# Performance work log

Hardware: AMD Instinct MI355X
Metric: run time of the kernel (lower is better)

Reference implementation:

```python
import jax, jax.numpy as jnp
import numpy as np


def setup_inputs() -> dict:
    key = jax.random.key(0)
    ks = jax.random.split(key, 6)
    B_, S, D_in, D_out, R, E = 4, 2048, 2048, 2048, 64, 16
    x = jax.random.normal(ks[0], (B_, S, D_in), dtype=jnp.float32)
    W_base = jax.random.normal(ks[1], (D_out, D_in), dtype=jnp.float32) * (D_in ** -0.5)
    b_base = jax.random.normal(ks[2], (D_out,), dtype=jnp.float32) * 0.02
    # orthogonal rows, as get_orthogonal_matrix(reservoir_size, in_features)
    G = np.asarray(jax.random.normal(ks[3], (D_in, R), dtype=jnp.float32))
    Q, _ = np.linalg.qr(G)  # [D_in, R] orthonormal columns
    A = jnp.asarray(Q.T, dtype=jnp.float32)  # [R, D_in]
    # B initialized to zeros in the module; use small random so delta is nontrivial
    Bmat = jax.random.normal(ks[4], (E, D_out, R), dtype=jnp.float32) * 0.02
    W_router = jax.random.normal(ks[5], (E, D_in), dtype=jnp.float32) * 0.02
    return {"x": x, "W_base": W_base, "b_base": b_base, "A": A, "B": Bmat,
            "W_router": W_router, "top_k": 2}


def reference(x, W_base, b_base, A, B, W_router, top_k):
    E = W_router.shape[0]
    base_output = jnp.einsum('bsi,oi->bso', x, W_base) + b_base          # [B,S,D_out]
    res_hidden = jnp.einsum('bsi,ri->bsr', x, A)                          # [B,S,R]
    router_logits = jnp.einsum('bsi,ei->bse', x, W_router)                # [B,S,E]
    routing_weights = jax.nn.softmax(router_logits, axis=-1)
    if top_k > 0 and top_k < E:
        _, top_idx = jax.lax.top_k(routing_weights, top_k)                # [B,S,k]
        mask = jax.nn.one_hot(top_idx, E, dtype=routing_weights.dtype).sum(axis=-2)
        routing_weights = routing_weights * mask
        routing_weights = routing_weights / (routing_weights.sum(axis=-1, keepdims=True) + 1e-6)
    # contract experts+rank without materializing [B,S,E,D_out]
    h = jnp.einsum('bsr,bse->bser', res_hidden, routing_weights)          # [B,S,E,R] (small)
    delta = jnp.einsum('bser,edr->bsd', h, B)                             # [B,S,D_out]
    return base_output + delta
```

## Files before the change

### kernel.cpp

```cpp
#include <hip/hip_runtime.h>
#include <hip/hip_bf16.h>

#define D_IN  2048
#define D_OUT 2048
#define RNK   64
#define NE    16
#define KTOT  3072

typedef __attribute__((ext_vector_type(8))) short bf16x8;
typedef __attribute__((ext_vector_type(4))) float f32x4;

__device__ __forceinline__ void async_ld16(const void* g, void* l) {
    __builtin_amdgcn_global_load_lds(
        (const __attribute__((address_space(1))) void*)g,
        (__attribute__((address_space(3))) void*)l,
        16, 0, 0);
}

__global__ __launch_bounds__(384) void castwa_kernel(
    const float* __restrict__ Wb, const float* __restrict__ Bm,
    const float* __restrict__ A,
    __hip_bfloat16* __restrict__ Wc, __hip_bfloat16* __restrict__ Ab)
{
    const int c = threadIdx.x * 8;
    const float* src;
    __hip_bfloat16* dst;
    if (blockIdx.x < D_OUT) {
        const int n = blockIdx.x;
        if (c < D_IN) {
            src = Wb + (size_t)n * D_IN + c;
        } else {
            const int j = c - D_IN;
            const int e = j >> 6, r = j & 63;
            src = Bm + ((size_t)e * D_OUT + n) * RNK + r;
        }
        dst = Wc + (size_t)n * KTOT + c;
    } else {
        if (c >= D_IN) return;
        const int r = blockIdx.x - D_OUT;
        src = A + (size_t)r * D_IN + c;
        dst = Ab + (size_t)r * D_IN + c;
    }
    const float4 a = *(const float4*)src;
    const float4 b = *(const float4*)(src + 4);
    const float vv[8] = {a.x, a.y, a.z, a.w, b.x, b.y, b.z, b.w};
    union { bf16x8 v; __hip_bfloat16 h[8]; } u;
#pragma unroll
    for (int q = 0; q < 8; ++q) u.h[q] = __float2bfloat16(vv[q]);
    *(bf16x8*)dst = u.v;
}

__global__ __launch_bounds__(256) void prep_kernel(
    const float* __restrict__ x, const float* __restrict__ Wr,
    const int* __restrict__ topk_p, __hip_bfloat16* __restrict__ Xc,
    float* __restrict__ wfin)
{
    __shared__ __align__(16) float wr_lds[2][NE * 256];
    const int tid = threadIdx.x;
    const int wave = tid >> 6, lane = tid & 63;
    const int t0 = blockIdx.x * 8 + wave * 2;

    float acc[NE][2];
#pragma unroll
    for (int e = 0; e < NE; ++e) { acc[e][0] = 0.f; acc[e][1] = 0.f; }

    const float4* x4 = (const float4*)x;

    auto stage = [&](int buf, int i) {
#pragma unroll
        for (int j = 0; j < 4; ++j) {
            const int r = wave * 4 + j;
            async_ld16(Wr + (size_t)r * D_IN + i * 256 + lane * 4,
                       (void*)&wr_lds[buf][r * 256]);
        }
    };

    stage(0, 0);
    __syncthreads();

#pragma unroll
    for (int i = 0; i < 8; ++i) {
        if (i < 7) stage((i + 1) & 1, i + 1);

        float4 xv[2];
#pragma unroll
        for (int t = 0; t < 2; ++t) {
            xv[t] = x4[(size_t)(t0 + t) * 512 + i * 64 + lane];
            union { short4 v; __hip_bfloat16 h[4]; } u;
            u.h[0] = __float2bfloat16(xv[t].x); u.h[1] = __float2bfloat16(xv[t].y);
            u.h[2] = __float2bfloat16(xv[t].z); u.h[3] = __float2bfloat16(xv[t].w);
            *(short4*)(Xc + (size_t)(t0 + t) * KTOT + (i * 64 + lane) * 4) = u.v;
        }

        const float4* wr4 = (const float4*)wr_lds[i & 1];
#pragma unroll
        for (int e = 0; e < NE; ++e) {
            const float4 wv = wr4[e * 64 + lane];
#pragma unroll
            for (int t = 0; t < 2; ++t)
                acc[e][t] += xv[t].x * wv.x + xv[t].y * wv.y
                           + xv[t].z * wv.z + xv[t].w * wv.w;
        }
        __syncthreads();
    }

#pragma unroll
    for (int off = 32; off; off >>= 1)
#pragma unroll
        for (int e = 0; e < NE; ++e)
#pragma unroll
            for (int t = 0; t < 2; ++t)
                acc[e][t] += __shfl_xor(acc[e][t], off, 64);

    if (lane < 2) {
        const int tt = lane;
        const int k = topk_p[0];
        float m = -1e30f;
#pragma unroll
        for (int e = 0; e < NE; ++e) m = fmaxf(m, acc[e][tt]);
        float w[NE]; float ssum = 0.f;
#pragma unroll
        for (int e = 0; e < NE; ++e) { w[e] = __expf(acc[e][tt] - m); ssum += w[e]; }
        const float inv = 1.f / ssum;
#pragma unroll
        for (int e = 0; e < NE; ++e) w[e] *= inv;
        float* wfout = wfin + (size_t)(t0 + tt) * NE;
        if (k > 0 && k < NE) {
            int chosen[NE];
#pragma unroll
            for (int e = 0; e < NE; ++e) chosen[e] = 0;
            float ksum = 0.f;
            for (int it = 0; it < k; ++it) {
                int bi = 0; float bv = -1.f;
                for (int e = 0; e < NE; ++e)
                    if (!chosen[e] && w[e] > bv) { bv = w[e]; bi = e; }
                chosen[bi] = 1; ksum += bv;
            }
            const float rinv = 1.f / (ksum + 1e-6f);
            for (int e = 0; e < NE; ++e) wfout[e] = chosen[e] ? w[e] * rinv : 0.f;
        } else {
            for (int e = 0; e < NE; ++e) wfout[e] = w[e];
        }
    }
}

__global__ __launch_bounds__(256) void rhfused_kernel(
    __hip_bfloat16* Xc, const __hip_bfloat16* __restrict__ Ab,
    const float* __restrict__ wfin)
{
    __shared__ __align__(16) char smem[10240 + 1024];
    __hip_bfloat16* lds_a = (__hip_bfloat16*)smem;
    __hip_bfloat16* lds_b = (__hip_bfloat16*)(smem + 2048);
    const int tid = threadIdx.x;
    const int wave = tid >> 6, lane = tid & 63;
    const int qm = lane & 15, quad = lane >> 4;
    const int ar = lane >> 3;
    const int ac = ((lane & 7) ^ ar) * 8;
    const int t0b = blockIdx.x * 16;

    f32x4 acc = {};

    for (int k0 = 0; k0 < D_IN; k0 += 64) {
        if (wave < 2) {
            const __hip_bfloat16* ga =
                Xc + (size_t)(t0b + wave * 8 + ar) * KTOT + k0 + ac;
            async_ld16(ga, (void*)&lds_a[wave * 512]);
        }
#pragma unroll
        for (int j = 0; j < 2; ++j) {
            const __hip_bfloat16* gb =
                Ab + (size_t)(wave * 16 + j * 8 + ar) * D_IN + k0 + ac;
            async_ld16(gb, (void*)&lds_b[(wave * 2 + j) * 512]);
        }
        __syncthreads();
#pragma unroll
        for (int kk = 0; kk < 64; kk += 32) {
            const int cg = (kk >> 3) + quad;
            const int sw = (cg ^ (qm & 7)) * 8;
            bf16x8 af = *(const bf16x8*)&lds_a[qm * 64 + sw];
            bf16x8 bfr = *(const bf16x8*)&lds_b[(wave * 16 + qm) * 64 + sw];
            acc = __builtin_amdgcn_mfma_f32_16x16x32_bf16(af, bfr, acc, 0, 0, 0);
        }
        __syncthreads();
    }

    float* rh = (float*)smem;
    float* wf = (float*)(smem + 4096);
#pragma unroll
    for (int r = 0; r < 4; ++r)
        rh[(quad * 4 + r) * 64 + wave * 16 + qm] = acc[r];
    if (tid < 64) {
        const int t = tid >> 2, part = tid & 3;
        ((float4*)wf)[t * 4 + part] =
            ((const float4*)(wfin + (size_t)(t0b + t) * NE))[part];
    }
    __syncthreads();

#pragma unroll
    for (int it = 0; it < 8; ++it) {
        const int s = it * 256 + tid;
        const int t = s >> 7;
        const int chunk = s & 127;
        const int e = chunk >> 3, r0 = (chunk & 7) * 8;
        const float w = wf[t * 16 + e];
        union { bf16x8 v; __hip_bfloat16 h[8]; } u;
#pragma unroll
        for (int q = 0; q < 8; ++q)
            u.h[q] = __float2bfloat16(w * rh[t * 64 + r0 + q]);
        *(bf16x8*)(Xc + (size_t)(t0b + t) * KTOT + D_IN + chunk * 8) = u.v;
    }
}

__global__ __launch_bounds__(256) void gemm_kernel(
    const __hip_bfloat16* __restrict__ Am,
    const __hip_bfloat16* __restrict__ Bm,
    const float* __restrict__ bias,
    float* __restrict__ C, int M, int N)
{
    __shared__ __hip_bfloat16 lds_a[128 * 64];
    __shared__ __hip_bfloat16 lds_b[128 * 64];
    const int tid = threadIdx.x;
    const int wave = tid >> 6, lane = tid & 63;
    const int bm = blockIdx.x, bn = blockIdx.y;
    const int qm = lane & 15, quad = lane >> 4;
    const int ar = lane >> 3;
    const int ac = ((lane & 7) ^ ar) * 8;

    f32x4 acc[4][4] = {};
    const int wm = (wave >> 1) * 64, wn = (wave & 1) * 64;

    const __hip_bfloat16* ga[4];
    const __hip_bfloat16* gb[4];
#pragma unroll
    for (int j = 0; j < 4; ++j) {
        ga[j] = Am + (size_t)(bm * 128 + wave * 32 + j * 8 + ar) * KTOT + ac;
        gb[j] = Bm + (size_t)(bn * 128 + wave * 32 + j * 8 + ar) * KTOT + ac;
    }

    for (int k0 = 0; k0 < KTOT; k0 += 64) {
#pragma unroll
        for (int j = 0; j < 4; ++j) {
            async_ld16(ga[j], (void*)&lds_a[(wave * 4 + j) * 512]);
            async_ld16(gb[j], (void*)&lds_b[(wave * 4 + j) * 512]);
            ga[j] += 64; gb[j] += 64;
        }
        __syncthreads();

#pragma unroll
        for (int kk = 0; kk < 64; kk += 32) {
            const int cg = (kk >> 3) + quad;
            const int sw = (cg ^ (qm & 7)) * 8;
            bf16x8 af[4], bfr[4];
#pragma unroll
            for (int i = 0; i < 4; ++i)
                af[i] = *(const bf16x8*)&lds_a[(wm + i * 16 + qm) * 64 + sw];
#pragma unroll
            for (int j = 0; j < 4; ++j)
                bfr[j] = *(const bf16x8*)&lds_b[(wn + j * 16 + qm) * 64 + sw];
#pragma unroll
            for (int i = 0; i < 4; ++i)
#pragma unroll
                for (int j = 0; j < 4; ++j)
                    acc[i][j] = __builtin_amdgcn_mfma_f32_16x16x32_bf16(
                        af[i], bfr[j], acc[i][j], 0, 0, 0);
        }
        __syncthreads();
    }

    const size_t row0 = (size_t)bm * 128 + wm;
    const int col0 = bn * 128 + wn;
#pragma unroll
    for (int j = 0; j < 4; ++j) {
        const int col = col0 + j * 16 + qm;
        const float bb = bias[col];
#pragma unroll
        for (int i = 0; i < 4; ++i) {
#pragma unroll
            for (int r = 0; r < 4; ++r) {
                const size_t row = row0 + i * 16 + quad * 4 + r;
                C[row * (size_t)N + col] = acc[i][j][r] + bb;
            }
        }
    }
}

extern "C" void kernel_launch(void* const* d_in, const int* in_sizes, int n_in,
                              void* d_out, int out_size, void* d_ws, size_t ws_size,
                              hipStream_t stream) {
    const float* x    = (const float*)d_in[0];
    const float* Wb   = (const float*)d_in[1];
    const float* bb   = (const float*)d_in[2];
    const float* A    = (const float*)d_in[3];
    const float* Bm   = (const float*)d_in[4];
    const float* Wr   = (const float*)d_in[5];
    const int*   topk = (const int*)d_in[6];
    float* out = (float*)d_out;
    const int T = in_sizes[0] / D_IN;

    __hip_bfloat16* Xc = (__hip_bfloat16*)d_ws;
    __hip_bfloat16* Wc = (__hip_bfloat16*)((char*)d_ws + (size_t)T * KTOT * 2);
    __hip_bfloat16* Ab = (__hip_bfloat16*)d_out;
    float* wfin = (float*)d_out + 8 * 1024 * 1024;

    castwa_kernel<<<D_OUT + RNK, 384, 0, stream>>>(Wb, Bm, A, Wc, Ab);
    prep_kernel<<<T / 8, 256, 0, stream>>>(x, Wr, topk, Xc, wfin);
    rhfused_kernel<<<T / 16, 256, 0, stream>>>(Xc, Ab, wfin);
    gemm_kernel<<<dim3(T / 128, D_OUT / 128), 256, 0, stream>>>(Xc, Wc, bb, out, T, D_OUT);
}
```

Before: 302.4 us.

## Split-K rh kernel across waves with direct global loads and LDS reduction

The res_hidden kernel now gives each wave a quarter of the K dimension and has it compute all 64 rank columns. Operands are loaded straight from global memory into registers, replacing the async LDS staging and the two barriers per K step. The four partial results are then summed through LDS before the routing weights are applied. This removes most synchronisation and gives more MFMA work per load, at the cost of more register pressure and uncoalesced 16-byte global reads of the A matrix by every block.

```diff
diff --git a/kernel.cpp b/kernel.cpp
--- a/kernel.cpp
+++ b/kernel.cpp
@@ -148,52 +148,45 @@
     __hip_bfloat16* Xc, const __hip_bfloat16* __restrict__ Ab,
     const float* __restrict__ wfin)
 {
-    __shared__ __align__(16) char smem[10240 + 1024];
-    __hip_bfloat16* lds_a = (__hip_bfloat16*)smem;
-    __hip_bfloat16* lds_b = (__hip_bfloat16*)(smem + 2048);
+    __shared__ __align__(16) float red[4][16][64];
+    __shared__ __align__(16) float wf[16 * 16];
     const int tid = threadIdx.x;
     const int wave = tid >> 6, lane = tid & 63;
     const int qm = lane & 15, quad = lane >> 4;
-    const int ar = lane >> 3;
-    const int ac = ((lane & 7) ^ ar) * 8;
-    const int t0b = blockIdx.x * 16;
-
-    f32x4 acc = {};
-
-    for (int k0 = 0; k0 < D_IN; k0 += 64) {
-        if (wave < 2) {
-            const __hip_bfloat16* ga =
-                Xc + (size_t)(t0b + wave * 8 + ar) * KTOT + k0 + ac;
-            async_ld16(ga, (void*)&lds_a[wave * 512]);
-        }
-#pragma unroll
-        for (int j = 0; j < 2; ++j) {
-            const __hip_bfloat16* gb =
-                Ab + (size_t)(wave * 16 + j * 8 + ar) * D_IN + k0 + ac;
-            async_ld16(gb, (void*)&lds_b[(wave * 2 + j) * 512]);
-        }
-        __syncthreads();
-#pragma unroll
-        for (int kk = 0; kk < 64; kk += 32) {
-            const int cg = (kk >> 3) + quad;
-            const int sw = (cg ^ (qm & 7)) * 8;
-            bf16x8 af = *(const bf16x8*)&lds_a[qm * 64 + sw];
-            bf16x8 bfr = *(const bf16x8*)&lds_b[(wave * 16 + qm) * 64 + sw];
-            acc = __builtin_amdgcn_mfma_f32_16x16x32_bf16(af, bfr, acc, 0, 0, 0);
-        }
-        __syncthreads();
-    }
-
-    float* rh = (float*)smem;
-    float* wf = (float*)(smem + 4096);
-#pragma unroll
-    for (int r = 0; r < 4; ++r)
-        rh[(quad * 4 + r) * 64 + wave * 16 + qm] = acc[r];
-    if (tid < 64) {
-        const int t = tid >> 2, part = tid & 3;
-        ((float4*)wf)[t * 4 + part] =
-            ((const float4*)(wfin + (size_t)(t0b + t) * NE))[part];
-    }
+    const int t0 = blockIdx.x * 16;
+
+    const __hip_bfloat16* xrow =
+        Xc + (size_t)(t0 + qm) * KTOT + wave * 512 + quad * 8;
+    const __hip_bfloat16* brow =
+        Ab + (size_t)qm * D_IN + wave * 512 + quad * 8;
+
+    f32x4 acc[4] = {};
+#pragma unroll
+    for (int s = 0; s < 8; ++s) {
+        const bf16x8 a0 = *(const bf16x8*)(xrow);
+        const bf16x8 a1 = *(const bf16x8*)(xrow + 32);
+        bf16x8 b0[4], b1[4];
+#pragma unroll
+        for (int nf = 0; nf < 4; ++nf) {
+            b0[nf] = *(const bf16x8*)(brow + (size_t)nf * 16 * D_IN);
+            b1[nf] = *(const bf16x8*)(brow + (size_t)nf * 16 * D_IN + 32);
+        }
+        xrow += 64; brow += 64;
+#pragma unroll
+        for (int nf = 0; nf < 4; ++nf) {
+            acc[nf] = __builtin_amdgcn_mfma_f32_16x16x32_bf16(a0, b0[nf], acc[nf], 0, 0, 0);
+            acc[nf] = __builtin_amdgcn_mfma_f32_16x16x32_bf16(a1, b1[nf], acc[nf], 0, 0, 0);
+        }
+    }
+
+#pragma unroll
+    for (int nf = 0; nf < 4; ++nf)
+#pragma unroll
+        for (int r = 0; r < 4; ++r)
+            red[wave][quad * 4 + r][nf * 16 + qm] = acc[nf][r];
+
+    if (tid < 64)
+        ((float4*)wf)[tid] = ((const float4*)(wfin + (size_t)t0 * NE))[tid];
     __syncthreads();
 
 #pragma unroll
@@ -205,9 +198,12 @@
         const float w = wf[t * 16 + e];
         union { bf16x8 v; __hip_bfloat16 h[8]; } u;
 #pragma unroll
-        for (int q = 0; q < 8; ++q)
-            u.h[q] = __float2bfloat16(w * rh[t * 64 + r0 + q]);
-        *(bf16x8*)(Xc + (size_t)(t0b + t) * KTOT + D_IN + chunk * 8) = u.v;
+        for (int q = 0; q < 8; ++q) {
+            const float rh = red[0][t][r0 + q] + red[1][t][r0 + q]
+                           + red[2][t][r0 + q] + red[3][t][r0 + q];
+            u.h[q] = __float2bfloat16(w * rh);
+        }
+        *(bf16x8*)(Xc + (size_t)(t0 + t) * KTOT + D_IN + chunk * 8) = u.v;
     }
 }
 
```

Result: no change. 305.7 us (+1.1%).
